# Optimization experiments

Hardware: AMD Instinct MI355X
Metric: run time of the kernel (lower is better)

## Reference

```python
import jax, jax.numpy as jnp
import numpy as np

EPS = 1e-5

def _layernorm(x, gamma, beta):
    mu = jnp.mean(x, axis=-1, keepdims=True)
    var = jnp.var(x, axis=-1, keepdims=True)
    return (x - mu) * jax.lax.rsqrt(var + EPS) * gamma + beta

def setup_inputs() -> dict:
    key = jax.random.key(0)
    ks = jax.random.split(key, 6)
    B, S, N, c_m, c_z, H, c = 1, 512, 384, 64, 128, 8, 32
    return {
        "m_si": jax.random.normal(ks[0], (B, S, N, c_m), dtype=jnp.float32),
        "z_ij": jax.random.normal(ks[1], (B, N, N, c_z), dtype=jnp.float32),
        "gamma_m": jnp.ones((c_m,), dtype=jnp.float32),
        "beta_m": jnp.zeros((c_m,), dtype=jnp.float32),
        "W1": jax.random.normal(ks[2], (c_m, c * H), dtype=jnp.float32) * 0.05,
        "gamma_z": jnp.ones((c_z,), dtype=jnp.float32),
        "beta_z": jnp.zeros((c_z,), dtype=jnp.float32),
        "W2": jax.random.normal(ks[3], (c_z, H), dtype=jnp.float32) * 0.05,
        "W3": jax.random.normal(ks[4], (c_m, c * H), dtype=jnp.float32) * 0.05,
        "W4": jax.random.normal(ks[5], (c * H, c_m), dtype=jnp.float32) * 0.05,
    }

def reference(m_si, z_ij, gamma_m, beta_m, W1, gamma_z, beta_z, W2, W3, W4):
    B, S, N, c_m = m_si.shape
    H = W2.shape[-1]
    c = W1.shape[-1] // H
    m = _layernorm(m_si, gamma_m, beta_m)                 # [B,S,N,c_m]
    v = (m @ W1).reshape(B, S, N, H, c)                   # values  [B,S,N,H,c]
    g = jax.nn.sigmoid(m @ W3).reshape(B, S, N, H, c)     # gates   [B,S,N,H,c]
    b = _layernorm(z_ij, gamma_z, beta_z) @ W2            # pair bias [B,i,j,H]
    # original: softmax over dim=-2 of [B,H,i,j] i.e. over the i axis
    w = jax.nn.softmax(b, axis=1)                         # [B,i,j,H]
    # broadcast weighted average over tokens, shared across N_msa
    o = g * jnp.einsum('bijh,bsjhc->bsihc', w, v)         # [B,S,N,H,c]
    return o.reshape(B, S, N, H * c) @ W4                 # [B,S,N,c_m]
```

## Files before the change

kernel.cpp:

```cpp
#include <hip/hip_runtime.h>
#include <hip/hip_bf16.h>
#include <math.h>


typedef __attribute__((ext_vector_type(8))) short bf16x8;
typedef __attribute__((ext_vector_type(4))) float f32x4;
typedef unsigned int u32;

__global__ __launch_bounds__(256) void k0_prep(
    const float* __restrict__ W4, const float* __restrict__ W1,
    const float* __restrict__ W3,
    __hip_bfloat16* __restrict__ W4t,
    __hip_bfloat16* __restrict__ W13s)
{
    int idx = blockIdx.x * 256 + threadIdx.x;
    if (idx < 16384) {
        int d = idx >> 8, k = idx & 255;
        W4t[idx] = __float2bfloat16(W4[k * 64 + d]);
    } else {
        int t = idx - 16384;
        int n = t >> 6, k = t & 63;
        float v = (n < 256) ? W1[k * 256 + n] : W3[k * 256 + (n - 256)];
        int dst = n * 64 + ((((k >> 3) ^ (n & 7))) << 3) + (k & 7);
        W13s[dst] = __float2bfloat16(v);
    }
}

__global__ __launch_bounds__(256) void k1_ln_mv(
    const float* __restrict__ m_si,
    const float* __restrict__ gamma_m, const float* __restrict__ beta_m,
    const __hip_bfloat16* __restrict__ W13s,
    __hip_bfloat16* __restrict__ v_tg,
    __hip_bfloat16* __restrict__ g_bf)
{
    __shared__ short a_t[128 * 64];
    __shared__ short b_t[512 * 64];
    const int bx = blockIdx.x;
    const int s = bx / 3, j0 = (bx % 3) * 128;
    const int tid = threadIdx.x;
    const int lane = tid & 63, wv = tid >> 6;
    const int col = lane & 15, quad = lane >> 4;

    {
        const short* src = (const short*)W13s;
        #pragma unroll
        for (int i = 0; i < 16; i++) {
            __builtin_amdgcn_global_load_lds(
                (const __attribute__((address_space(1))) u32*)
                    (src + i * 2048 + wv * 512 + lane * 8),
                (__attribute__((address_space(3))) u32*)(b_t + i * 2048 + wv * 512),
                16, 0, 0);
        }
    }

    {
        const float gm = gamma_m[lane], bm = beta_m[lane];
        const float* mrow = m_si + (size_t)(s * 384 + j0) * 64;
        const int cl = lane >> 3, e = lane & 7;
        #pragma unroll 4
        for (int rr = 0; rr < 32; rr++) {
            int r = wv * 32 + rr;
            float x = mrow[r * 64 + lane];
            float s1 = x, s2 = x * x;
            #pragma unroll
            for (int off = 32; off > 0; off >>= 1) {
                s1 += __shfl_xor(s1, off, 64);
                s2 += __shfl_xor(s2, off, 64);
            }
            float mu  = s1 * (1.0f / 64.0f);
            float var = s2 * (1.0f / 64.0f) - mu * mu;
            float rs  = rsqrtf(var + 1e-5f);
            __hip_bfloat16 mh = __float2bfloat16((x - mu) * rs * gm + bm);
            a_t[r * 64 + ((cl ^ (r & 7)) << 3) + e] = *(short*)&mh;
        }
    }
    __syncthreads();

    const int wm = wv >> 1, wn = wv & 1;

    bf16x8 mf[4][2];
    #pragma unroll
    for (int mt = 0; mt < 4; mt++) {
        int r = wm * 64 + mt * 16 + col;
        #pragma unroll
        for (int ks = 0; ks < 2; ks++) {
            int c = ks * 4 + quad;
            mf[mt][ks] = *(const bf16x8*)&a_t[r * 64 + ((c ^ (r & 7)) << 3)];
        }
    }

    short* vbase = (short*)v_tg + (size_t)s * 98304;
    __hip_bfloat16* gb = g_bf + (size_t)s * 98304;

    #pragma unroll 1
    for (int step = 0; step < 4; step++) {
        bf16x8 wf[4][2];
        #pragma unroll
        for (int nt = 0; nt < 4; nt++) {
            int n = step * 128 + wn * 64 + nt * 16 + col;
            #pragma unroll
            for (int ks = 0; ks < 2; ks++) {
                int c = ks * 4 + quad;
                wf[nt][ks] = *(const bf16x8*)&b_t[n * 64 + ((c ^ (n & 7)) << 3)];
            }
        }

        if (step < 2) {
            f32x4 acc[4][4];
            #pragma unroll
            for (int nt = 0; nt < 4; nt++)
                #pragma unroll
                for (int mt = 0; mt < 4; mt++)
                    acc[nt][mt] = (f32x4){0.f, 0.f, 0.f, 0.f};
            #pragma unroll
            for (int ks = 0; ks < 2; ks++)
                #pragma unroll
                for (int nt = 0; nt < 4; nt++)
                    #pragma unroll
                    for (int mt = 0; mt < 4; mt++)
                        acc[nt][mt] = __builtin_amdgcn_mfma_f32_16x16x32_bf16(
                            wf[nt][ks], mf[mt][ks], acc[nt][mt], 0, 0, 0);
            #pragma unroll
            for (int nt = 0; nt < 4; nt++)
                #pragma unroll
                for (int mt = 0; mt < 4; mt++) {
                    int jg = j0 + wm * 64 + mt * 16 + col;
                    #pragma unroll
                    for (int reg = 0; reg < 4; reg++) {
                        int n = step * 128 + wn * 64 + nt * 16 + quad * 4 + reg;
                        __hip_bfloat16 t = __float2bfloat16(acc[nt][mt][reg]);
                        vbase[n * 384 + jg] = *(short*)&t;
                    }
                }
        } else {
            f32x4 acc[4][4];
            #pragma unroll
            for (int mt = 0; mt < 4; mt++)
                #pragma unroll
                for (int nt = 0; nt < 4; nt++)
                    acc[mt][nt] = (f32x4){0.f, 0.f, 0.f, 0.f};
            #pragma unroll
            for (int ks = 0; ks < 2; ks++)
                #pragma unroll
                for (int mt = 0; mt < 4; mt++)
                    #pragma unroll
                    for (int nt = 0; nt < 4; nt++)
                        acc[mt][nt] = __builtin_amdgcn_mfma_f32_16x16x32_bf16(
                            mf[mt][ks], wf[nt][ks], acc[mt][nt], 0, 0, 0);
            #pragma unroll
            for (int mt = 0; mt < 4; mt++)
                #pragma unroll
                for (int nt = 0; nt < 4; nt++) {
                    int n = (step - 2) * 128 + wn * 64 + nt * 16 + col;
                    #pragma unroll
                    for (int reg = 0; reg < 4; reg++) {
                        int jg = j0 + wm * 64 + mt * 16 + quad * 4 + reg;
                        float gv = 1.0f / (1.0f + __expf(-acc[mt][nt][reg]));
                        gb[(size_t)jg * 256 + n] = __float2bfloat16(gv);
                    }
                }
        }
    }
}

__global__ __launch_bounds__(256) void k2_ln_z(
    const float* __restrict__ z,
    const float* __restrict__ gamma_z, const float* __restrict__ beta_z,
    const float* __restrict__ W2, float* __restrict__ b_buf)
{
    const int tid = threadIdx.x;
    const int lane = tid & 63, wv = tid >> 6;
    const int R0 = blockIdx.x * 64;
    __shared__ float part[64][9];

    float2 g2 = *(const float2*)&gamma_z[lane * 2];
    float2 be2 = *(const float2*)&beta_z[lane * 2];
    float4 w2a = *(const float4*)&W2[lane * 16];
    float4 w2b = *(const float4*)&W2[lane * 16 + 4];
    float4 w2c = *(const float4*)&W2[lane * 16 + 8];
    float4 w2d = *(const float4*)&W2[lane * 16 + 12];

    const bool hi4 = (lane & 4) != 0;
    const bool hi2 = (lane & 2) != 0;
    const bool hi1 = (lane & 1) != 0;

    float2 zx = *(const float2*)&z[(size_t)(R0 + wv * 16) * 128 + lane * 2];
    #pragma unroll 1
    for (int rr = 0; rr < 16; rr++) {
        const int rl = wv * 16 + rr;
        float x0 = zx.x, x1 = zx.y;
        if (rr < 15)
            zx = *(const float2*)&z[(size_t)(R0 + rl + 1) * 128 + lane * 2];

        float s1 = x0 + x1, s2 = x0 * x0 + x1 * x1;
        #pragma unroll
        for (int off = 32; off > 0; off >>= 1) {
            s1 += __shfl_xor(s1, off, 64);
            s2 += __shfl_xor(s2, off, 64);
        }
        float mu  = s1 * (1.0f / 128.0f);
        float var = s2 * (1.0f / 128.0f) - mu * mu;
        float rs  = rsqrtf(var + 1e-5f);
        float mh0 = (x0 - mu) * rs * g2.x + be2.x;
        float mh1 = (x1 - mu) * rs * g2.y + be2.y;

        float p[8];
        p[0] = fmaf(mh0, w2a.x, mh1 * w2c.x);
        p[1] = fmaf(mh0, w2a.y, mh1 * w2c.y);
        p[2] = fmaf(mh0, w2a.z, mh1 * w2c.z);
        p[3] = fmaf(mh0, w2a.w, mh1 * w2c.w);
        p[4] = fmaf(mh0, w2b.x, mh1 * w2d.x);
        p[5] = fmaf(mh0, w2b.y, mh1 * w2d.y);
        p[6] = fmaf(mh0, w2b.z, mh1 * w2d.z);
        p[7] = fmaf(mh0, w2b.w, mh1 * w2d.w);

        float t[4];
        #pragma unroll
        for (int k = 0; k < 4; k++) {
            float keep = hi4 ? p[k + 4] : p[k];
            float send = hi4 ? p[k] : p[k + 4];
            t[k] = keep + __shfl_xor(send, 4, 64);
        }
        float u[2];
        #pragma unroll
        for (int k = 0; k < 2; k++) {
            float keep = hi2 ? t[k + 2] : t[k];
            float send = hi2 ? t[k] : t[k + 2];
            u[k] = keep + __shfl_xor(send, 2, 64);
        }
        float vsum;
        {
            float keep = hi1 ? u[1] : u[0];
            float send = hi1 ? u[0] : u[1];
            vsum = keep + __shfl_xor(send, 1, 64);
        }
        vsum += __shfl_xor(vsum, 8, 64);
        vsum += __shfl_xor(vsum, 16, 64);
        vsum += __shfl_xor(vsum, 32, 64);
        if (lane < 8) part[rl][lane] = vsum;
    }
    __syncthreads();

    {
        int h0 = tid >> 6, rl = tid & 63;
        b_buf[(size_t)h0 * 147456 + R0 + rl]       = part[rl][h0];
        b_buf[(size_t)(h0 + 4) * 147456 + R0 + rl] = part[rl][h0 + 4];
    }
}

__global__ __launch_bounds__(128) void k3a_part(
    const float* __restrict__ w_buf, float* __restrict__ pm, float* __restrict__ pl)
{
    const int h = blockIdx.x / 24, ic = blockIdx.x % 24;
    const int i0 = ic * 16;
    const int tid = threadIdx.x;
    const float* base = w_buf + ((size_t)h * 384 + i0) * 384;

    float m0 = -INFINITY, m1 = -INFINITY, m2 = -INFINITY;
    float l0 = 0.f, l1 = 0.f, l2 = 0.f;
    #pragma unroll 4
    for (int ii = 0; ii < 16; ii++) {
        float x0 = base[ii * 384 + tid];
        float x1 = base[ii * 384 + tid + 128];
        float x2 = base[ii * 384 + tid + 256];
        float n0 = fmaxf(m0, x0);
        l0 = l0 * __expf(m0 - n0) + __expf(x0 - n0); m0 = n0;
        float n1 = fmaxf(m1, x1);
        l1 = l1 * __expf(m1 - n1) + __expf(x1 - n1); m1 = n1;
        float n2 = fmaxf(m2, x2);
        l2 = l2 * __expf(m2 - n2) + __expf(x2 - n2); m2 = n2;
    }
    float* pmb = pm + ((size_t)h * 24 + ic) * 384;
    float* plb = pl + ((size_t)h * 24 + ic) * 384;
    pmb[tid]       = m0;  plb[tid]       = l0;
    pmb[tid + 128] = m1;  plb[tid + 128] = l1;
    pmb[tid + 256] = m2;  plb[tid + 256] = l2;
}

__global__ __launch_bounds__(384) void k3m_comb(
    const float* __restrict__ pm, const float* __restrict__ pl,
    float* __restrict__ Mf, float* __restrict__ invLf)
{
    const int h = blockIdx.x, j = threadIdx.x;
    float M = -INFINITY, L = 0.f;
    #pragma unroll 4
    for (int ic = 0; ic < 24; ic++) {
        float m = pm[((size_t)h * 24 + ic) * 384 + j];
        float l = pl[((size_t)h * 24 + ic) * 384 + j];
        float nM = fmaxf(M, m);
        L = L * __expf(M - nM) + l * __expf(m - nM);
        M = nM;
    }
    Mf[h * 384 + j] = M;
    invLf[h * 384 + j] = 1.0f / L;
}

__global__ __launch_bounds__(128) void k3b_write(
    const float* __restrict__ w_buf, const float* __restrict__ Mf,
    const float* __restrict__ invLf, __hip_bfloat16* __restrict__ w_bf)
{
    const int h = blockIdx.x / 24, ic = blockIdx.x % 24;
    const int i0 = ic * 16;
    const int tid = threadIdx.x;
    const float* base = w_buf + ((size_t)h * 384 + i0) * 384;
    __hip_bfloat16* ob = w_bf + ((size_t)h * 384 + i0) * 384;

    float M0 = Mf[h * 384 + tid],       iL0 = invLf[h * 384 + tid];
    float M1 = Mf[h * 384 + tid + 128], iL1 = invLf[h * 384 + tid + 128];
    float M2 = Mf[h * 384 + tid + 256], iL2 = invLf[h * 384 + tid + 256];
    #pragma unroll 4
    for (int ii = 0; ii < 16; ii++) {
        float x0 = base[ii * 384 + tid];
        float x1 = base[ii * 384 + tid + 128];
        float x2 = base[ii * 384 + tid + 256];
        ob[ii * 384 + tid]       = __float2bfloat16(__expf(x0 - M0) * iL0);
        ob[ii * 384 + tid + 128] = __float2bfloat16(__expf(x1 - M1) * iL1);
        ob[ii * 384 + tid + 256] = __float2bfloat16(__expf(x2 - M2) * iL2);
    }
}

#define OSTR 264

__global__ __launch_bounds__(256, 2) void k4_mfma(
    const __hip_bfloat16* __restrict__ w_bf,
    const __hip_bfloat16* __restrict__ v_tg,
    const __hip_bfloat16* __restrict__ g_bf,
    const __hip_bfloat16* __restrict__ W4t,
    float* __restrict__ out)
{
    __shared__ short v_t[2][6144];
    __shared__ short o_l[64 * OSTR];
    const int bx0 = blockIdx.x;
    const int bx = (bx0 & 7) * 384 + (bx0 >> 3);
    const int s = bx / 6, i0 = (bx % 6) * 64;
    const int tid = threadIdx.x;
    const int lane = tid & 63, wv = tid >> 6;
    const int col = lane & 15, quad = lane >> 4;
    const int swz = col & 7;

    int srow[3], skc[3];
    #pragma unroll
    for (int r = 0; r < 3; r++) {
        int p = r * 256 + tid;
        int row = p / 48;
        srow[r] = row;
        skc[r] = (p - row * 48) ^ (row & 7);
    }

    const short* wA_base = (const short*)w_bf
        + (size_t)(i0 + wv * 16 + col) * 384 + quad * 8;
    const short* vslab = (const short*)v_tg + (size_t)s * 98304;
    const __hip_bfloat16* gbase = g_bf + (size_t)(s * 384 + i0) * 256;
    const int ibase = wv * 16 + quad * 4;

    auto STAGE = [&](int buf, int h, int half) {
        const short* src = vslab + h * 12288 + half * 6144;
        short* dstb = &v_t[buf][wv * 512];
        #pragma unroll
        for (int r = 0; r < 3; r++) {
            __builtin_amdgcn_global_load_lds(
                (const __attribute__((address_space(1))) u32*)
                    (src + srow[r] * 384 + skc[r] * 8),
                (__attribute__((address_space(3))) u32*)(dstb + r * 2048),
                16, 0, 0);
        }
    };

    auto COMPUTE = [&](int buf, int h) -> f32x4 {
        f32x4 acc = {0.f, 0.f, 0.f, 0.f};
        const short* wA = wA_base + (size_t)h * 147456;
        #pragma unroll
        for (int ks = 0; ks < 12; ks++) {
            int k0 = ks * 32;
            bf16x8 a = *(const bf16x8*)(wA + k0);
            int ch = (ks * 4 + quad) ^ swz;
            bf16x8 b = *(const bf16x8*)&v_t[buf][col * 384 + ch * 8];
            acc = __builtin_amdgcn_mfma_f32_16x16x32_bf16(a, b, acc, 0, 0, 0);
        }
        return acc;
    };

    STAGE(0, 0, 0);
    __syncthreads();

    int cur = 0;
    #pragma unroll 1
    for (int h = 0; h < 8; h++) {
        STAGE(cur ^ 1, h, 1);
        float g0[4], g1[4];
        #pragma unroll
        for (int reg = 0; reg < 4; reg++) {
            int il = ibase + reg;
            g0[reg] = __bfloat162float(gbase[il * 256 + h * 32 + col]);
            g1[reg] = __bfloat162float(gbase[il * 256 + h * 32 + 16 + col]);
        }
        f32x4 acc0 = COMPUTE(cur, h);
        __syncthreads();
        cur ^= 1;

        if (h < 7) STAGE(cur ^ 1, h + 1, 0);
        f32x4 acc1 = COMPUTE(cur, h);
        #pragma unroll
        for (int reg = 0; reg < 4; reg++) {
            int il = ibase + reg;
            __hip_bfloat16 t0 = __float2bfloat16(acc0[reg] * g0[reg]);
            __hip_bfloat16 t1 = __float2bfloat16(acc1[reg] * g1[reg]);
            o_l[il * OSTR + h * 32 + col]      = *(short*)&t0;
            o_l[il * OSTR + h * 32 + 16 + col] = *(short*)&t1;
        }
        __syncthreads();
        cur ^= 1;
    }

    f32x4 acc2[4];
    #pragma unroll
    for (int n = 0; n < 4; n++) acc2[n] = (f32x4){0.f, 0.f, 0.f, 0.f};
    #pragma unroll
    for (int ks = 0; ks < 8; ks++) {
        int k0 = ks * 32;
        bf16x8 a = *(const bf16x8*)&o_l[(wv * 16 + col) * OSTR + k0 + quad * 8];
        #pragma unroll
        for (int n = 0; n < 4; n++) {
            bf16x8 b = *(const bf16x8*)((const short*)W4t
                        + (n * 16 + col) * 256 + k0 + quad * 8);
            acc2[n] = __builtin_amdgcn_mfma_f32_16x16x32_bf16(a, b, acc2[n], 0, 0, 0);
        }
    }
    float* obase = out + (size_t)(s * 384 + i0 + wv * 16 + quad * 4) * 64;
    #pragma unroll
    for (int n = 0; n < 4; n++)
        #pragma unroll
        for (int reg = 0; reg < 4; reg++)
            obase[reg * 64 + n * 16 + col] = acc2[n][reg];
}

extern "C" void kernel_launch(void* const* d_in, const int* in_sizes, int n_in,
                              void* d_out, int out_size, void* d_ws, size_t ws_size,
                              hipStream_t stream)
{
    const float* m_si    = (const float*)d_in[0];
    const float* z_ij    = (const float*)d_in[1];
    const float* gamma_m = (const float*)d_in[2];
    const float* beta_m  = (const float*)d_in[3];
    const float* W1      = (const float*)d_in[4];
    const float* gamma_z = (const float*)d_in[5];
    const float* beta_z  = (const float*)d_in[6];
    const float* W2      = (const float*)d_in[7];
    const float* W3      = (const float*)d_in[8];
    const float* W4      = (const float*)d_in[9];
    float* out = (float*)d_out;

    char* ws = (char*)d_ws;
    __hip_bfloat16* g_bf = (__hip_bfloat16*)ws;
    __hip_bfloat16* v_tg = (__hip_bfloat16*)(ws + 100663296);
    float*          w_buf = (float*)(ws + 201326592);
    __hip_bfloat16* W13s = (__hip_bfloat16*)(ws + 201326592);
    __hip_bfloat16* w_bf = (__hip_bfloat16*)(ws + 206045184);
    __hip_bfloat16* W4t  = (__hip_bfloat16*)(ws + 208404480);
    float* pm    = (float*)(ws + 208437248);
    float* pl    = (float*)(ws + 208732160);
    float* Mf    = (float*)(ws + 209027072);
    float* invLf = (float*)(ws + 209039360);

    k0_prep  <<<192,  256, 0, stream>>>(W4, W1, W3, W4t, W13s);
    k1_ln_mv <<<1536, 256, 0, stream>>>(m_si, gamma_m, beta_m, W13s, v_tg, g_bf);
    k2_ln_z  <<<2304, 256, 0, stream>>>(z_ij, gamma_z, beta_z, W2, w_buf);
    k3a_part <<<192,  128, 0, stream>>>(w_buf, pm, pl);
    k3m_comb <<<8,    384, 0, stream>>>(pm, pl, Mf, invLf);
    k3b_write<<<192,  128, 0, stream>>>(w_buf, Mf, invLf, w_bf);
    k4_mfma  <<<3072, 256, 0, stream>>>(w_bf, v_tg, g_bf, W4t, out);
}
```

Baseline: 511.4 us.

## Triple-buffer V staging with manual vmcnt waits and reuse A fragments per head

The LDS buffer for V tiles grows from double to triple buffering. Staging is issued one half-tile further ahead, and the explicit __syncthreads are replaced by s_waitcnt vmcnt plus s_barrier. The 12 w_bf A fragments are now loaded once per head into registers and shared by both half computations, where before they were reloaded from global memory for each half. The aim is to hide global-to-LDS latency and cut redundant global loads, at the cost of more LDS, more registers, and fragile hand-counted vmcnt ordering.

```diff
diff --git a/kernel.cpp b/kernel.cpp
--- a/kernel.cpp
+++ b/kernel.cpp
@@ -328,7 +328,7 @@
     const __hip_bfloat16* __restrict__ W4t,
     float* __restrict__ out)
 {
-    __shared__ short v_t[2][6144];
+    __shared__ short v_t[3][6144];
     __shared__ short o_l[64 * OSTR];
     const int bx0 = blockIdx.x;
     const int bx = (bx0 & 7) * 384 + (bx0 >> 3);
@@ -353,8 +353,8 @@
     const __hip_bfloat16* gbase = g_bf + (size_t)(s * 384 + i0) * 256;
     const int ibase = wv * 16 + quad * 4;
 
-    auto STAGE = [&](int buf, int h, int half) {
-        const short* src = vslab + h * 12288 + half * 6144;
+    auto STAGE = [&](int buf, int hh, int half) {
+        const short* src = vslab + hh * 12288 + half * 6144;
         short* dstb = &v_t[buf][wv * 512];
         #pragma unroll
         for (int r = 0; r < 3; r++) {
@@ -366,27 +366,40 @@
         }
     };
 
-    auto COMPUTE = [&](int buf, int h) -> f32x4 {
-        f32x4 acc = {0.f, 0.f, 0.f, 0.f};
-        const short* wA = wA_base + (size_t)h * 147456;
-        #pragma unroll
-        for (int ks = 0; ks < 12; ks++) {
-            int k0 = ks * 32;
-            bf16x8 a = *(const bf16x8*)(wA + k0);
-            int ch = (ks * 4 + quad) ^ swz;
-            bf16x8 b = *(const bf16x8*)&v_t[buf][col * 384 + ch * 8];
-            acc = __builtin_amdgcn_mfma_f32_16x16x32_bf16(a, b, acc, 0, 0, 0);
-        }
-        return acc;
-    };
-
     STAGE(0, 0, 0);
-    __syncthreads();
-
-    int cur = 0;
+    STAGE(1, 0, 1);
+
+    int cb = 0;
+    int sb = 2;
+
     #pragma unroll 1
     for (int h = 0; h < 8; h++) {
-        STAGE(cur ^ 1, h, 1);
+        asm volatile("s_waitcnt vmcnt(3)" ::: "memory");
+        __builtin_amdgcn_s_barrier();
+        __builtin_amdgcn_sched_barrier(0);
+
+        bf16x8 af[12];
+        const short* wA = wA_base + (size_t)h * 147456;
+        #pragma unroll
+        for (int ks = 0; ks < 12; ks++)
+            af[ks] = *(const bf16x8*)(wA + ks * 32);
+
+        if (h < 7) { STAGE(sb, h + 1, 0); sb = (sb == 2) ? 0 : sb + 1; }
+
+        f32x4 acc0 = {0.f, 0.f, 0.f, 0.f};
+        #pragma unroll
+        for (int ks = 0; ks < 12; ks++) {
+            int ch = (ks * 4 + quad) ^ swz;
+            bf16x8 b = *(const bf16x8*)&v_t[cb][col * 384 + ch * 8];
+            acc0 = __builtin_amdgcn_mfma_f32_16x16x32_bf16(af[ks], b, acc0, 0, 0, 0);
+        }
+        cb = (cb == 2) ? 0 : cb + 1;
+
+        if (h < 7) asm volatile("s_waitcnt vmcnt(3)" ::: "memory");
+        else       asm volatile("s_waitcnt vmcnt(0)" ::: "memory");
+        __builtin_amdgcn_s_barrier();
+        __builtin_amdgcn_sched_barrier(0);
+
         float g0[4], g1[4];
         #pragma unroll
         for (int reg = 0; reg < 4; reg++) {
@@ -394,12 +407,18 @@
             g0[reg] = __bfloat162float(gbase[il * 256 + h * 32 + col]);
             g1[reg] = __bfloat162float(gbase[il * 256 + h * 32 + 16 + col]);
         }
-        f32x4 acc0 = COMPUTE(cur, h);
-        __syncthreads();
-        cur ^= 1;
-
-        if (h < 7) STAGE(cur ^ 1, h + 1, 0);
-        f32x4 acc1 = COMPUTE(cur, h);
+
+        if (h < 7) { STAGE(sb, h + 1, 1); sb = (sb == 2) ? 0 : sb + 1; }
+
+        f32x4 acc1 = {0.f, 0.f, 0.f, 0.f};
+        #pragma unroll
+        for (int ks = 0; ks < 12; ks++) {
+            int ch = (ks * 4 + quad) ^ swz;
+            bf16x8 b = *(const bf16x8*)&v_t[cb][col * 384 + ch * 8];
+            acc1 = __builtin_amdgcn_mfma_f32_16x16x32_bf16(af[ks], b, acc1, 0, 0, 0);
+        }
+        cb = (cb == 2) ? 0 : cb + 1;
+
         #pragma unroll
         for (int reg = 0; reg < 4; reg++) {
             int il = ibase + reg;
@@ -408,8 +427,6 @@
             o_l[il * OSTR + h * 32 + col]      = *(short*)&t0;
             o_l[il * OSTR + h * 32 + 16 + col] = *(short*)&t1;
         }
-        __syncthreads();
-        cur ^= 1;
     }
 
     f32x4 acc2[4];
```

Result: slower. 524.5 us (+2.6%).
